# Optimization experiments

Measured on AMD Instinct MI355X. Metric: run time of the kernel, lower is better.

The kernel has to match this reference:

```python
import jax, jax.numpy as jnp
import numpy as np

B, T, D = 2, 2048, 2048
H = 16
D_HEAD = D // H          # 128
D_SUB = D_HEAD // 2      # 64
SCALE = float(np.sqrt(D_SUB))


def setup_inputs() -> dict:
    key = jax.random.key(0)
    ks = jax.random.split(key, 6)
    s = 1.0 / np.sqrt(D)
    return {
        "x": jax.random.normal(ks[0], (B, T, D), dtype=jnp.float32),
        "W_q": jax.random.normal(ks[1], (D, D), dtype=jnp.float32) * s,
        "W_k": jax.random.normal(ks[2], (D, D), dtype=jnp.float32) * s,
        "W_v": jax.random.normal(ks[3], (D, D), dtype=jnp.float32) * s,
        "W_o": jax.random.normal(ks[4], (D, D), dtype=jnp.float32) * s,
        "lambda_param": jnp.full((H,), 0.8, dtype=jnp.float32),
    }


def reference(x, W_q, W_k, W_v, W_o, lambda_param):
    # Linear layers (torch nn.Linear: x @ W.T), reshape to heads
    Q = (x @ W_q.T).reshape(B, T, H, D_HEAD)
    K = (x @ W_k.T).reshape(B, T, H, D_HEAD)
    V = (x @ W_v.T).reshape(B, T, H, D_HEAD)
    # split each head into two sub-heads
    Q1, Q2 = Q[..., :D_SUB], Q[..., D_SUB:2 * D_SUB]
    K1, K2 = K[..., :D_SUB], K[..., D_SUB:2 * D_SUB]
    # dual attention maps: [B, H, T, T]
    attn1 = jnp.einsum('bthd,bshd->bhts', Q1, K1) / SCALE
    attn2 = jnp.einsum('bthd,bshd->bhts', Q2, K2) / SCALE
    A1 = jax.nn.softmax(attn1, axis=-1)
    A2 = jax.nn.softmax(attn2, axis=-1)
    lam = jax.nn.sigmoid(lambda_param)[None, :, None, None]  # [1,H,1,1]
    A_diff = A1 - lam * A2
    # weighted values -> [B, T, H, d_head] -> [B, T, D]
    out = jnp.einsum('bhts,bshd->bthd', A_diff, V).reshape(B, T, D)
    return out @ W_o.T
```

## Files before the change

kernel.cpp:

```cpp
#include <hip/hip_runtime.h>
#include <math.h>

#define B_  2
#define T_  2048
#define D_  2048
#define H_  16
#define DH  128
#define BT  (B_ * T_)

typedef float    f32x4 __attribute__((ext_vector_type(4)));
typedef _Float16 f16x8 __attribute__((ext_vector_type(8)));

typedef __attribute__((address_space(1))) const void* gas_t;
typedef __attribute__((address_space(3))) void*       las_t;

__device__ __forceinline__ void gll16(const void* g, void* l) {
    __builtin_amdgcn_global_load_lds((gas_t)g, (las_t)l, 16, 0, 0);
}

__device__ __forceinline__ unsigned short h16bits(float f) {
    union { _Float16 h; unsigned short u; } c; c.h = (_Float16)f; return c.u;
}

__global__ __launch_bounds__(256)
void f32_to_f16(const float* __restrict__ in, _Float16* __restrict__ out, int n8) {
    int i = blockIdx.x * 256 + threadIdx.x;
    if (i >= n8) return;
    const float4 a = *(const float4*)(in + (size_t)i * 8);
    const float4 b = *(const float4*)(in + (size_t)i * 8 + 4);
    f16x8 o;
    o[0] = (_Float16)a.x; o[1] = (_Float16)a.y; o[2] = (_Float16)a.z; o[3] = (_Float16)a.w;
    o[4] = (_Float16)b.x; o[5] = (_Float16)b.y; o[6] = (_Float16)b.z; o[7] = (_Float16)b.w;
    *(f16x8*)(out + (size_t)i * 8) = o;
}

#define BKK 64

template<int EPI>
__global__ __launch_bounds__(256, 2)
void gemm16(const _Float16* __restrict__ Ag, const _Float16* __restrict__ Bg,
            float* __restrict__ Cf, _Float16* __restrict__ C16,
            _Float16* __restrict__ Vt, int M, int N, int K) {
    __shared__ _Float16 As[128 * BKK];
    __shared__ _Float16 Bs[128 * BKK];

    const int tid  = threadIdx.x;
    const int lane = tid & 63;
    const int w    = tid >> 6;
    const int wr   = w >> 1, wc = w & 1;
    const int c    = lane & 15, g = lane >> 4;

    const int nwg = gridDim.x;
    const int bid = blockIdx.x;
    const int swz = (bid & 7) * (nwg >> 3) + (bid >> 3);
    const int nb  = N / 128;
    const int bm  = (swz / nb) * 128;
    const int bn  = (swz % nb) * 128;

    const int srow = tid >> 3;
    const int sg   = (tid & 7) ^ (srow & 7);
    const _Float16* Ab = Ag + (size_t)(bm + srow) * K + sg * 8;
    const _Float16* Bb = Bg + (size_t)(bn + srow) * K + sg * 8;

    f32x4 acc[4][4];
    #pragma unroll
    for (int mi = 0; mi < 4; ++mi)
        #pragma unroll
        for (int ni = 0; ni < 4; ++ni)
            #pragma unroll
            for (int r = 0; r < 4; ++r) acc[mi][ni][r] = 0.f;

    for (int k0 = 0; k0 < K; k0 += BKK) {
        __syncthreads();
        #pragma unroll
        for (int i = 0; i < 4; ++i) {
            gll16(Ab + (size_t)i * 32 * K + k0, &As[(i * 256 + tid) * 8]);
            gll16(Bb + (size_t)i * 32 * K + k0, &Bs[(i * 256 + tid) * 8]);
        }
        __syncthreads();

        #pragma unroll
        for (int kc = 0; kc < 2; ++kc) {
            f16x8 fa[4], fb[4];
            #pragma unroll
            for (int mi = 0; mi < 4; ++mi) {
                const int row = wr * 64 + mi * 16 + c;
                fa[mi] = *(const f16x8*)&As[row * 64 + (((kc * 4 + g) ^ (c & 7)) * 8)];
            }
            #pragma unroll
            for (int ni = 0; ni < 4; ++ni) {
                const int row = wc * 64 + ni * 16 + c;
                fb[ni] = *(const f16x8*)&Bs[row * 64 + (((kc * 4 + g) ^ (c & 7)) * 8)];
            }
            #pragma unroll
            for (int mi = 0; mi < 4; ++mi)
                #pragma unroll
                for (int ni = 0; ni < 4; ++ni)
                    acc[mi][ni] = __builtin_amdgcn_mfma_f32_16x16x32_f16(fa[mi], fb[ni], acc[mi][ni], 0, 0, 0);
        }
    }

    #pragma unroll
    for (int mi = 0; mi < 4; ++mi) {
        #pragma unroll
        for (int ni = 0; ni < 4; ++ni) {
            const int m0 = bm + wr * 64 + mi * 16 + g * 4;
            const int n  = bn + wc * 64 + ni * 16 + c;
            if constexpr (EPI == 0) {
                #pragma unroll
                for (int r = 0; r < 4; ++r)
                    Cf[(size_t)(m0 + r) * N + n] = acc[mi][ni][r];
            } else if constexpr (EPI == 1) {
                #pragma unroll
                for (int r = 0; r < 4; ++r)
                    C16[(size_t)(m0 + r) * N + n] = (_Float16)acc[mi][ni][r];
            } else {
                const int bb = m0 >> 11, t = m0 & (T_ - 1);
                ushort4 o;
                o.x = h16bits(acc[mi][ni][0]); o.y = h16bits(acc[mi][ni][1]);
                o.z = h16bits(acc[mi][ni][2]); o.w = h16bits(acc[mi][ni][3]);
                *(ushort4*)&Vt[((size_t)bb * D_ + n) * T_ + t] = o;
            }
        }
    }
}

__device__ __forceinline__ void softmax_upd(f32x4 s[4], f32x4 O[8],
                                            float& m, float& l,
                                            unsigned pk[4][2], int g) {
    float tmax = -1e30f;
    #pragma unroll
    for (int mt = 0; mt < 4; ++mt)
        #pragma unroll
        for (int r = 0; r < 4; ++r) {
            s[mt][r] *= 0.125f;
            tmax = fmaxf(tmax, s[mt][r]);
        }
    tmax = fmaxf(tmax, __shfl_xor(tmax, 16));
    tmax = fmaxf(tmax, __shfl_xor(tmax, 32));
    if (!__all(tmax <= m + 8.f)) {
        float mnew = fmaxf(m, tmax);
        float al   = __expf(m - mnew);
        #pragma unroll
        for (int r = 0; r < 4; ++r) {
            float alr = __shfl(al, (g << 2) | r);
            #pragma unroll
            for (int nt = 0; nt < 8; ++nt) O[nt][r] *= alr;
        }
        l *= al;
        m  = mnew;
    }
    float tsum = 0.f;
    #pragma unroll
    for (int mt = 0; mt < 4; ++mt)
        #pragma unroll
        for (int r = 0; r < 4; ++r) {
            float p = __expf(s[mt][r] - m);
            s[mt][r] = p; tsum += p;
        }
    tsum += __shfl_xor(tsum, 16);
    tsum += __shfl_xor(tsum, 32);
    l += tsum;
    #pragma unroll
    for (int mt = 0; mt < 4; ++mt) {
        pk[mt][0] = (unsigned)h16bits(s[mt][0]) | ((unsigned)h16bits(s[mt][1]) << 16);
        pk[mt][1] = (unsigned)h16bits(s[mt][2]) | ((unsigned)h16bits(s[mt][3]) << 16);
    }
}

__global__ __launch_bounds__(256, 2)
void diff_attn_f16(_Float16* Qh,
                   const _Float16* __restrict__ Kh,
                   const _Float16* __restrict__ Vt,
                   const float* __restrict__ lambda_param) {
    __shared__ _Float16 k_s[2][64 * 128];
    __shared__ _Float16 v_s[2][128 * 64];

    const int tid  = threadIdx.x;
    const int lane = tid & 63;
    const int w    = tid >> 6;
    const int b    = blockIdx.z, h = blockIdx.y;
    const int t0   = blockIdx.x * 64;
    const int c    = lane & 15;
    const int g    = lane >> 4;

    const float lam = 1.f / (1.f + __expf(-lambda_param[h]));

    const int q0 = t0 + w * 16;
    const _Float16* Qg = Qh + (size_t)(b * T_ + q0 + c) * D_ + h * DH;
    f16x8 qf[4];
    #pragma unroll
    for (int kb = 0; kb < 4; ++kb)
        qf[kb] = *(const f16x8*)&Qg[kb * 32 + g * 8];

    f32x4 O1[8], O2[8];
    #pragma unroll
    for (int nt = 0; nt < 8; ++nt)
        #pragma unroll
        for (int r = 0; r < 4; ++r) { O1[nt][r] = 0.f; O2[nt][r] = 0.f; }
    float m1 = -1e30f, l1 = 0.f, m2 = -1e30f, l2 = 0.f;

    const int kkey = tid >> 4;
    const int kgs  = (tid & 15) ^ (kkey & 7);
    const int vd   = tid >> 3;
    const int vgs  = (tid & 7) ^ (vd & 7);
    const size_t rowK = (size_t)(b * T_);
    const size_t rowV = (size_t)(b * D_ + h * DH);

    auto STAGE = [&](int s0, int buf) {
        #pragma unroll
        for (int i = 0; i < 4; ++i) {
            const size_t goff = (rowK + s0 + i * 16 + kkey) * (size_t)D_ + h * DH + kgs * 8;
            gll16(&Kh[goff], &k_s[buf][(i * 256 + tid) * 8]);
        }
        #pragma unroll
        for (int i = 0; i < 4; ++i) {
            const size_t goff = (rowV + i * 32 + vd) * (size_t)T_ + s0 + vgs * 8;
            gll16(&Vt[goff], &v_s[buf][(i * 256 + tid) * 8]);
        }
    };

    STAGE(0, 0);
    __syncthreads();

    const int NT = T_ / 64;
    for (int t = 0; t < NT; ++t) {
        const int cur = t & 1;
        if (t + 1 < NT) STAGE((t + 1) * 64, cur ^ 1);

        f32x4 s1[4], s2[4];
        #pragma unroll
        for (int mt = 0; mt < 4; ++mt)
            #pragma unroll
            for (int r = 0; r < 4; ++r) { s1[mt][r] = 0.f; s2[mt][r] = 0.f; }
        #pragma unroll
        for (int mt = 0; mt < 4; ++mt) {
            const int key  = mt * 16 + c;
            const int krow = key * 128;
            #pragma unroll
            for (int kb = 0; kb < 4; ++kb) {
                const int gp = ((4 * kb + g) ^ (key & 7)) * 8;
                f16x8 kf = *(const f16x8*)&k_s[cur][krow + gp];
                if (kb < 2) s1[mt] = __builtin_amdgcn_mfma_f32_16x16x32_f16(kf, qf[kb], s1[mt], 0, 0, 0);
                else        s2[mt] = __builtin_amdgcn_mfma_f32_16x16x32_f16(kf, qf[kb], s2[mt], 0, 0, 0);
            }
        }

        unsigned pk1[4][2], pk2[4][2];
        softmax_upd(s1, O1, m1, l1, pk1, g);
        softmax_upd(s2, O2, m2, l2, pk2, g);

        const int srcA = ((2 * (g & 1)) << 4) | c;
        const int srcB = ((2 * (g & 1) + 1) << 4) | c;
        const bool hiSel = (g & 2) != 0;
        #pragma unroll
        for (int kb = 0; kb < 2; ++kb) {
            f16x8 vf[8];
            #pragma unroll
            for (int nt = 0; nt < 8; ++nt) {
                const int d  = nt * 16 + c;
                const int gp = ((4 * kb + g) ^ (d & 7)) * 8;
                vf[nt] = *(const f16x8*)&v_s[cur][d * 64 + gp];
            }
            unsigned u00 = (unsigned)__shfl((int)pk1[2 * kb][0], srcA);
            unsigned u10 = (unsigned)__shfl((int)pk1[2 * kb + 1][0], srcA);
            unsigned u01 = (unsigned)__shfl((int)pk1[2 * kb][1], srcA);
            unsigned u11 = (unsigned)__shfl((int)pk1[2 * kb + 1][1], srcA);
            unsigned u02 = (unsigned)__shfl((int)pk1[2 * kb][0], srcB);
            unsigned u12 = (unsigned)__shfl((int)pk1[2 * kb + 1][0], srcB);
            unsigned u03 = (unsigned)__shfl((int)pk1[2 * kb][1], srcB);
            unsigned u13 = (unsigned)__shfl((int)pk1[2 * kb + 1][1], srcB);
            union { unsigned u[4]; f16x8 v; } pa1;
            pa1.u[0] = hiSel ? u10 : u00;
            pa1.u[1] = hiSel ? u11 : u01;
            pa1.u[2] = hiSel ? u12 : u02;
            pa1.u[3] = hiSel ? u13 : u03;
            unsigned w00 = (unsigned)__shfl((int)pk2[2 * kb][0], srcA);
            unsigned w10 = (unsigned)__shfl((int)pk2[2 * kb + 1][0], srcA);
            unsigned w01 = (unsigned)__shfl((int)pk2[2 * kb][1], srcA);
            unsigned w11 = (unsigned)__shfl((int)pk2[2 * kb + 1][1], srcA);
            unsigned w02 = (unsigned)__shfl((int)pk2[2 * kb][0], srcB);
            unsigned w12 = (unsigned)__shfl((int)pk2[2 * kb + 1][0], srcB);
            unsigned w03 = (unsigned)__shfl((int)pk2[2 * kb][1], srcB);
            unsigned w13 = (unsigned)__shfl((int)pk2[2 * kb + 1][1], srcB);
            union { unsigned u[4]; f16x8 v; } pa2;
            pa2.u[0] = hiSel ? w10 : w00;
            pa2.u[1] = hiSel ? w11 : w01;
            pa2.u[2] = hiSel ? w12 : w02;
            pa2.u[3] = hiSel ? w13 : w03;
            #pragma unroll
            for (int nt = 0; nt < 8; ++nt) {
                O1[nt] = __builtin_amdgcn_mfma_f32_16x16x32_f16(pa1.v, vf[nt], O1[nt], 0, 0, 0);
                O2[nt] = __builtin_amdgcn_mfma_f32_16x16x32_f16(pa2.v, vf[nt], O2[nt], 0, 0, 0);
            }
        }
        __syncthreads();
    }

    float il1[4], il2[4];
    #pragma unroll
    for (int r = 0; r < 4; ++r) {
        float L1 = __shfl(l1, (g << 2) | r);
        float L2 = __shfl(l2, (g << 2) | r);
        il1[r] = 1.f / L1;
        il2[r] = lam / L2;
    }
    const size_t obase = (size_t)(b * T_ + q0) * D_ + h * DH;
    #pragma unroll
    for (int nt = 0; nt < 8; ++nt)
        #pragma unroll
        for (int r = 0; r < 4; ++r) {
            float o = O1[nt][r] * il1[r] - O2[nt][r] * il2[r];
            Qh[obase + (size_t)(g * 4 + r) * D_ + nt * 16 + c] = (_Float16)o;
        }
}

extern "C" void kernel_launch(void* const* d_in, const int* in_sizes, int n_in,
                              void* d_out, int out_size, void* d_ws, size_t ws_size,
                              hipStream_t stream) {
    const float* x    = (const float*)d_in[0];
    const float* W_q  = (const float*)d_in[1];
    const float* W_k  = (const float*)d_in[2];
    const float* W_v  = (const float*)d_in[3];
    const float* W_o  = (const float*)d_in[4];
    const float* lamp = (const float*)d_in[5];
    float* out = (float*)d_out;

    const size_t PL = (size_t)BT * D_;
    const size_t WL = (size_t)D_ * D_;
    _Float16* Xh = (_Float16*)d_ws;
    _Float16* Wq = Xh + PL;
    _Float16* Wk = Wq + WL;
    _Float16* Wv = Wk + WL;
    _Float16* Qh = Wv + WL;
    _Float16* Kh = Qh + PL;
    _Float16* Vt = Kh + PL;
    _Float16* Wo = Wq;

    f32_to_f16<<<(int)(PL / 8 / 256), 256, 0, stream>>>(x,   Xh, (int)(PL / 8));
    f32_to_f16<<<(int)(WL / 8 / 256), 256, 0, stream>>>(W_q, Wq, (int)(WL / 8));
    f32_to_f16<<<(int)(WL / 8 / 256), 256, 0, stream>>>(W_k, Wk, (int)(WL / 8));
    f32_to_f16<<<(int)(WL / 8 / 256), 256, 0, stream>>>(W_v, Wv, (int)(WL / 8));

    dim3 gg(512);
    gemm16<1><<<gg, 256, 0, stream>>>(Xh, Wq, nullptr, Qh, nullptr, BT, D_, D_);
    gemm16<1><<<gg, 256, 0, stream>>>(Xh, Wk, nullptr, Kh, nullptr, BT, D_, D_);
    gemm16<2><<<gg, 256, 0, stream>>>(Xh, Wv, nullptr, nullptr, Vt, BT, D_, D_);

    f32_to_f16<<<(int)(WL / 8 / 256), 256, 0, stream>>>(W_o, Wo, (int)(WL / 8));

    dim3 ga(T_ / 64, H_, B_);
    diff_attn_f16<<<ga, 256, 0, stream>>>(Qh, Kh, Vt, lamp);

    gemm16<0><<<gg, 256, 0, stream>>>(Qh, Wo, out, nullptr, nullptr, BT, D_, D_);
}
```

Baseline: 366.0 us.

## Enlarge attention blocks, use exp2 softmax, batch fp16 conversions, tune occupancy

The attention kernel now runs 512-thread blocks covering 128 queries, so each K/V tile staged in shared memory serves twice as many queries. Softmax folds log2(e) into the scale and uses exp2f, packs P with cvt_pkrtz, and raises wave priority around the MFMA sections. The four input fp32-to-fp16 conversions become one multi-tensor launch, and the GEMM launch bounds request three blocks per CU. Each of these carries its own risk: higher register pressure from the occupancy hints, pkrtz rounding toward zero, and idle blocks in the multi-convert grid for the smaller weight tensors.

```diff
diff --git a/kernel.cpp b/kernel.cpp
--- a/kernel.cpp
+++ b/kernel.cpp
@@ -10,6 +10,7 @@
 
 typedef float    f32x4 __attribute__((ext_vector_type(4)));
 typedef _Float16 f16x8 __attribute__((ext_vector_type(8)));
+typedef __fp16   fp16x2 __attribute__((ext_vector_type(2)));
 
 typedef __attribute__((address_space(1))) const void* gas_t;
 typedef __attribute__((address_space(3))) void*       las_t;
@@ -20,6 +21,33 @@
 
 __device__ __forceinline__ unsigned short h16bits(float f) {
     union { _Float16 h; unsigned short u; } c; c.h = (_Float16)f; return c.u;
+}
+__device__ __forceinline__ unsigned pk2h(float a, float b) {
+    union { fp16x2 h; unsigned u; } c;
+    c.h = __builtin_amdgcn_cvt_pkrtz(a, b);
+    return c.u;
+}
+
+__global__ __launch_bounds__(256)
+void f32_to_f16_multi(const float* __restrict__ s0, _Float16* __restrict__ d0, int n0,
+                      const float* __restrict__ s1, _Float16* __restrict__ d1, int n1,
+                      const float* __restrict__ s2, _Float16* __restrict__ d2, int n2,
+                      const float* __restrict__ s3, _Float16* __restrict__ d3, int n3) {
+    const float* s; _Float16* d; int n;
+    switch (blockIdx.y) {
+        case 0:  s = s0; d = d0; n = n0; break;
+        case 1:  s = s1; d = d1; n = n1; break;
+        case 2:  s = s2; d = d2; n = n2; break;
+        default: s = s3; d = d3; n = n3; break;
+    }
+    int i = blockIdx.x * 256 + threadIdx.x;
+    if (i >= n) return;
+    const float4 a = *(const float4*)(s + (size_t)i * 8);
+    const float4 b = *(const float4*)(s + (size_t)i * 8 + 4);
+    f16x8 o;
+    o[0] = (_Float16)a.x; o[1] = (_Float16)a.y; o[2] = (_Float16)a.z; o[3] = (_Float16)a.w;
+    o[4] = (_Float16)b.x; o[5] = (_Float16)b.y; o[6] = (_Float16)b.z; o[7] = (_Float16)b.w;
+    *(f16x8*)(d + (size_t)i * 8) = o;
 }
 
 __global__ __launch_bounds__(256)
@@ -37,7 +65,7 @@
 #define BKK 64
 
 template<int EPI>
-__global__ __launch_bounds__(256, 2)
+__global__ __launch_bounds__(256, 3)
 void gemm16(const _Float16* __restrict__ Ag, const _Float16* __restrict__ Bg,
             float* __restrict__ Cf, _Float16* __restrict__ C16,
             _Float16* __restrict__ Vt, int M, int N, int K) {
@@ -128,19 +156,20 @@
 __device__ __forceinline__ void softmax_upd(f32x4 s[4], f32x4 O[8],
                                             float& m, float& l,
                                             unsigned pk[4][2], int g) {
+    const float C1 = 0.125f * 1.44269504089f;
     float tmax = -1e30f;
     #pragma unroll
     for (int mt = 0; mt < 4; ++mt)
         #pragma unroll
         for (int r = 0; r < 4; ++r) {
-            s[mt][r] *= 0.125f;
+            s[mt][r] *= C1;
             tmax = fmaxf(tmax, s[mt][r]);
         }
     tmax = fmaxf(tmax, __shfl_xor(tmax, 16));
     tmax = fmaxf(tmax, __shfl_xor(tmax, 32));
     if (!__all(tmax <= m + 8.f)) {
         float mnew = fmaxf(m, tmax);
-        float al   = __expf(m - mnew);
+        float al   = exp2f(m - mnew);
         #pragma unroll
         for (int r = 0; r < 4; ++r) {
             float alr = __shfl(al, (g << 2) | r);
@@ -155,7 +184,7 @@
     for (int mt = 0; mt < 4; ++mt)
         #pragma unroll
         for (int r = 0; r < 4; ++r) {
-            float p = __expf(s[mt][r] - m);
+            float p = exp2f(s[mt][r] - m);
             s[mt][r] = p; tsum += p;
         }
     tsum += __shfl_xor(tsum, 16);
@@ -163,12 +192,12 @@
     l += tsum;
     #pragma unroll
     for (int mt = 0; mt < 4; ++mt) {
-        pk[mt][0] = (unsigned)h16bits(s[mt][0]) | ((unsigned)h16bits(s[mt][1]) << 16);
-        pk[mt][1] = (unsigned)h16bits(s[mt][2]) | ((unsigned)h16bits(s[mt][3]) << 16);
-    }
-}
-
-__global__ __launch_bounds__(256, 2)
+        pk[mt][0] = pk2h(s[mt][0], s[mt][1]);
+        pk[mt][1] = pk2h(s[mt][2], s[mt][3]);
+    }
+}
+
+__global__ __launch_bounds__(512, 4)
 void diff_attn_f16(_Float16* Qh,
                    const _Float16* __restrict__ Kh,
                    const _Float16* __restrict__ Vt,
@@ -180,7 +209,7 @@
     const int lane = tid & 63;
     const int w    = tid >> 6;
     const int b    = blockIdx.z, h = blockIdx.y;
-    const int t0   = blockIdx.x * 64;
+    const int t0   = blockIdx.x * 128;
     const int c    = lane & 15;
     const int g    = lane >> 4;
 
@@ -209,14 +238,14 @@
 
     auto STAGE = [&](int s0, int buf) {
         #pragma unroll
-        for (int i = 0; i < 4; ++i) {
-            const size_t goff = (rowK + s0 + i * 16 + kkey) * (size_t)D_ + h * DH + kgs * 8;
-            gll16(&Kh[goff], &k_s[buf][(i * 256 + tid) * 8]);
-        }
-        #pragma unroll
-        for (int i = 0; i < 4; ++i) {
-            const size_t goff = (rowV + i * 32 + vd) * (size_t)T_ + s0 + vgs * 8;
-            gll16(&Vt[goff], &v_s[buf][(i * 256 + tid) * 8]);
+        for (int i = 0; i < 2; ++i) {
+            const size_t goff = (rowK + s0 + i * 32 + kkey) * (size_t)D_ + h * DH + kgs * 8;
+            gll16(&Kh[goff], &k_s[buf][(i * 512 + tid) * 8]);
+        }
+        #pragma unroll
+        for (int i = 0; i < 2; ++i) {
+            const size_t goff = (rowV + i * 64 + vd) * (size_t)T_ + s0 + vgs * 8;
+            gll16(&Vt[goff], &v_s[buf][(i * 512 + tid) * 8]);
         }
     };
 
@@ -233,6 +262,7 @@
         for (int mt = 0; mt < 4; ++mt)
             #pragma unroll
             for (int r = 0; r < 4; ++r) { s1[mt][r] = 0.f; s2[mt][r] = 0.f; }
+        __builtin_amdgcn_s_setprio(1);
         #pragma unroll
         for (int mt = 0; mt < 4; ++mt) {
             const int key  = mt * 16 + c;
@@ -245,10 +275,11 @@
                 else        s2[mt] = __builtin_amdgcn_mfma_f32_16x16x32_f16(kf, qf[kb], s2[mt], 0, 0, 0);
             }
         }
-
-        unsigned pk1[4][2], pk2[4][2];
-        softmax_upd(s1, O1, m1, l1, pk1, g);
-        softmax_upd(s2, O2, m2, l2, pk2, g);
+        __builtin_amdgcn_s_setprio(0);
+
+        unsigned pk1[4][2], pk2v[4][2];
+        softmax_upd(s1, O1, m1, l1, pk1,  g);
+        softmax_upd(s2, O2, m2, l2, pk2v, g);
 
         const int srcA = ((2 * (g & 1)) << 4) | c;
         const int srcB = ((2 * (g & 1) + 1) << 4) | c;
@@ -275,24 +306,26 @@
             pa1.u[1] = hiSel ? u11 : u01;
             pa1.u[2] = hiSel ? u12 : u02;
             pa1.u[3] = hiSel ? u13 : u03;
-            unsigned w00 = (unsigned)__shfl((int)pk2[2 * kb][0], srcA);
-            unsigned w10 = (unsigned)__shfl((int)pk2[2 * kb + 1][0], srcA);
-            unsigned w01 = (unsigned)__shfl((int)pk2[2 * kb][1], srcA);
-            unsigned w11 = (unsigned)__shfl((int)pk2[2 * kb + 1][1], srcA);
-            unsigned w02 = (unsigned)__shfl((int)pk2[2 * kb][0], srcB);
-            unsigned w12 = (unsigned)__shfl((int)pk2[2 * kb + 1][0], srcB);
-            unsigned w03 = (unsigned)__shfl((int)pk2[2 * kb][1], srcB);
-            unsigned w13 = (unsigned)__shfl((int)pk2[2 * kb + 1][1], srcB);
+            unsigned w00 = (unsigned)__shfl((int)pk2v[2 * kb][0], srcA);
+            unsigned w10 = (unsigned)__shfl((int)pk2v[2 * kb + 1][0], srcA);
+            unsigned w01 = (unsigned)__shfl((int)pk2v[2 * kb][1], srcA);
+            unsigned w11 = (unsigned)__shfl((int)pk2v[2 * kb + 1][1], srcA);
+            unsigned w02 = (unsigned)__shfl((int)pk2v[2 * kb][0], srcB);
+            unsigned w12 = (unsigned)__shfl((int)pk2v[2 * kb + 1][0], srcB);
+            unsigned w03 = (unsigned)__shfl((int)pk2v[2 * kb][1], srcB);
+            unsigned w13 = (unsigned)__shfl((int)pk2v[2 * kb + 1][1], srcB);
             union { unsigned u[4]; f16x8 v; } pa2;
             pa2.u[0] = hiSel ? w10 : w00;
             pa2.u[1] = hiSel ? w11 : w01;
             pa2.u[2] = hiSel ? w12 : w02;
             pa2.u[3] = hiSel ? w13 : w03;
+            __builtin_amdgcn_s_setprio(1);
             #pragma unroll
             for (int nt = 0; nt < 8; ++nt) {
                 O1[nt] = __builtin_amdgcn_mfma_f32_16x16x32_f16(pa1.v, vf[nt], O1[nt], 0, 0, 0);
                 O2[nt] = __builtin_amdgcn_mfma_f32_16x16x32_f16(pa2.v, vf[nt], O2[nt], 0, 0, 0);
             }
+            __builtin_amdgcn_s_setprio(0);
         }
         __syncthreads();
     }
@@ -337,10 +370,11 @@
     _Float16* Vt = Kh + PL;
     _Float16* Wo = Wq;
 
-    f32_to_f16<<<(int)(PL / 8 / 256), 256, 0, stream>>>(x,   Xh, (int)(PL / 8));
-    f32_to_f16<<<(int)(WL / 8 / 256), 256, 0, stream>>>(W_q, Wq, (int)(WL / 8));
-    f32_to_f16<<<(int)(WL / 8 / 256), 256, 0, stream>>>(W_k, Wk, (int)(WL / 8));
-    f32_to_f16<<<(int)(WL / 8 / 256), 256, 0, stream>>>(W_v, Wv, (int)(WL / 8));
+    dim3 gc((unsigned)(PL / 8 + 255) / 256, 4);
+    f32_to_f16_multi<<<gc, 256, 0, stream>>>(x,   Xh, (int)(PL / 8),
+                                             W_q, Wq, (int)(WL / 8),
+                                             W_k, Wk, (int)(WL / 8),
+                                             W_v, Wv, (int)(WL / 8));
 
     dim3 gg(512);
     gemm16<1><<<gg, 256, 0, stream>>>(Xh, Wq, nullptr, Qh, nullptr, BT, D_, D_);
@@ -349,8 +383,8 @@
 
     f32_to_f16<<<(int)(WL / 8 / 256), 256, 0, stream>>>(W_o, Wo, (int)(WL / 8));
 
-    dim3 ga(T_ / 64, H_, B_);
-    diff_attn_f16<<<ga, 256, 0, stream>>>(Qh, Kh, Vt, lamp);
+    dim3 ga(T_ / 128, H_, B_);
+    diff_attn_f16<<<ga, 512, 0, stream>>>(Qh, Kh, Vt, lamp);
 
     gemm16<0><<<gg, 256, 0, stream>>>(Qh, Wo, out, nullptr, nullptr, BT, D_, D_);
 }
```

New measurement: 512.8 us. +40.1%, slower.
